# Kernel tuning notes

Hardware: AMD Instinct MI355X
Metric: run time of the kernel (lower is better)

## Reference

```python
import jax, jax.numpy as jnp
import numpy as np
import math

B, L, H = 2, 2048, 2048
NH, HD, RD = 16, 128, 64
QR, KVR = 768, 512


def rotate_half(x):
    d = x.shape[-1]
    x1, x2 = x[..., : d // 2], x[..., d // 2 :]
    return jnp.concatenate([-x2, x1], axis=-1)


def apply_rope(x):
    # x: [B, L, H, D] or [B, L, D]
    d = x.shape[-1]
    seq_len = x.shape[1]
    inv_freq = 1.0 / (10000.0 ** (jnp.arange(0, d, 2, dtype=x.dtype) / d))
    pos = jnp.arange(seq_len, dtype=x.dtype)
    freqs = jnp.outer(pos, inv_freq)  # [L, d/2]
    cos = jnp.concatenate([jnp.cos(freqs), jnp.cos(freqs)], axis=-1)  # [L, d]
    sin = jnp.concatenate([jnp.sin(freqs), jnp.sin(freqs)], axis=-1)
    if x.ndim == 4:
        cos, sin = cos[None, :, None, :], sin[None, :, None, :]
    else:
        cos, sin = cos[None, :, :], sin[None, :, :]
    return x * cos + rotate_half(x) * sin


def setup_inputs() -> dict:
    key = jax.random.key(0)
    ks = jax.random.split(key, 9)
    sc = lambda fan_in: 1.0 / math.sqrt(fan_in)
    return {
        "x": jax.random.normal(ks[0], (B, L, H), jnp.float32),
        "wq_down": jax.random.normal(ks[1], (H, QR), jnp.float32) * sc(H),
        "wq_up": jax.random.normal(ks[2], (QR, NH * HD), jnp.float32) * sc(QR),
        "wq_rope": jax.random.normal(ks[3], (QR, NH * RD), jnp.float32) * sc(QR),
        "wkv_down": jax.random.normal(ks[4], (H, KVR), jnp.float32) * sc(H),
        "wk_up": jax.random.normal(ks[5], (KVR, NH * HD), jnp.float32) * sc(KVR),
        "wv_up": jax.random.normal(ks[6], (KVR, NH * HD), jnp.float32) * sc(KVR),
        "wk_rope": jax.random.normal(ks[7], (H, RD), jnp.float32) * sc(H),
        "wo": jax.random.normal(ks[8], (NH * HD, H), jnp.float32) * sc(NH * HD),
    }


def reference(x, wq_down, wq_up, wq_rope, wkv_down, wk_up, wv_up, wk_rope, wo):
    b, l, _ = x.shape
    # Q low-rank path
    q_latent = x @ wq_down                              # [B,L,QR]
    q_content = (q_latent @ wq_up).reshape(b, l, NH, HD)
    q_rope = (q_latent @ wq_rope).reshape(b, l, NH, RD)
    q_rope = apply_rope(q_rope)
    # KV joint low-rank path
    kv_latent = x @ wkv_down                            # [B,L,KVR]
    k_content = (kv_latent @ wk_up).reshape(b, l, NH, HD)
    v = (kv_latent @ wv_up).reshape(b, l, NH, HD)
    # decoupled RoPE key (shared across heads)
    k_rope = apply_rope(x @ wk_rope)                    # [B,L,RD]
    k_rope = jnp.broadcast_to(k_rope[:, :, None, :], (b, l, NH, RD))
    q = jnp.concatenate([q_content, q_rope], axis=-1)   # [B,L,NH,HD+RD]
    k = jnp.concatenate([k_content, k_rope], axis=-1)
    scale = 1.0 / math.sqrt(HD + RD)
    scores = jnp.einsum("bqhd,bkhd->bhqk", q, k) * scale
    causal_mask = jnp.triu(jnp.ones((l, l), dtype=bool), k=1)
    scores = jnp.where(causal_mask[None, None], -jnp.inf, scores)
    attn = jax.nn.softmax(scores, axis=-1)
    out = jnp.einsum("bhqk,bkhd->bqhd", attn, v).reshape(b, l, NH * HD)
    return out @ wo
```

## Files before the change

### kernel.cpp

```cpp
#include <hip/hip_runtime.h>

typedef unsigned short u16;
typedef unsigned int u32;
typedef unsigned long long u64;
typedef __bf16 bf16x8 __attribute__((ext_vector_type(8)));
typedef float f32x4 __attribute__((ext_vector_type(4)));
typedef float f32x16 __attribute__((ext_vector_type(16)));
typedef u32 u32x4 __attribute__((ext_vector_type(4)));

#define DEV static __device__ __forceinline__

constexpr int B_ = 2, L_ = 2048, H_ = 2048;
constexpr int NH_ = 16, HD_ = 128, RD_ = 64;
constexpr int QR_ = 768, KVR_ = 512;
constexpr int BL_ = B_ * L_;
constexpr int QKD_ = HD_ + RD_;
constexpr int QKS_ = NH_ * QKD_;
constexpr int NHHD_ = NH_ * HD_;
constexpr int ROWS_ = B_ * NH_ * L_;
constexpr float SCALE2 = 0.07216878364870322f * 1.4426950408889634f;

DEV u16 f2bf(float f) {
    u32 u = __builtin_bit_cast(u32, f);
    u32 r = (u + 0x7fffu + ((u >> 16) & 1u)) >> 16;
    return (u16)r;
}
DEV float bf2f(u16 h) {
    u32 u = ((u32)h) << 16;
    return __builtin_bit_cast(float, u);
}
DEV u32 pk2(float lo, float hi) { return (u32)f2bf(lo) | ((u32)f2bf(hi) << 16); }
DEV bf16x8 ld8(const u16* p) { return __builtin_bit_cast(bf16x8, *(const u32x4*)p); }
DEV f32x4 mfma16(bf16x8 a, bf16x8 b, f32x4 c) {
    return __builtin_amdgcn_mfma_f32_16x16x32_bf16(a, b, c, 0, 0, 0);
}
DEV f32x16 mfma32(bf16x8 a, bf16x8 b, f32x16 c) {
    return __builtin_amdgcn_mfma_f32_32x32x16_bf16(a, b, c, 0, 0, 0);
}
DEV void gload16(const void* g, void* l) {
    __builtin_amdgcn_global_load_lds((const __attribute__((address_space(1))) void*)g,
                                     (__attribute__((address_space(3))) void*)l, 16, 0, 0);
}

__global__ __launch_bounds__(256) void cast_bf16_kernel(const float* __restrict__ src,
                                                        u16* __restrict__ dst, int n4) {
    int i = blockIdx.x * 256 + threadIdx.x;
    if (i >= n4) return;
    float4 v = ((const float4*)src)[i];
    u64 pk = (u64)f2bf(v.x) | ((u64)f2bf(v.y) << 16) | ((u64)f2bf(v.z) << 32) | ((u64)f2bf(v.w) << 48);
    ((u64*)dst)[i] = pk;
}

__global__ __launch_bounds__(256) void cast_transpose(const float* __restrict__ src, u16* __restrict__ dst,
                                                      int K, int N, int dstN) {
    __shared__ float tile[32][33];
    int n0 = blockIdx.x * 32, k0 = blockIdx.y * 32;
    int tx = threadIdx.x & 31, ty = threadIdx.x >> 5;
#pragma unroll
    for (int i = 0; i < 4; ++i) {
        int kk = ty + i * 8;
        int n = n0 + tx;
        tile[kk][tx] = (n < N) ? src[(size_t)(k0 + kk) * N + n] : 0.f;
    }
    __syncthreads();
#pragma unroll
    for (int i = 0; i < 4; ++i) {
        int nn = ty + i * 8;
        dst[(size_t)(n0 + nn) * K + k0 + tx] = f2bf(tile[tx][nn]);
    }
}

template <int OUTF32>
__global__ __launch_bounds__(256, 2) void gemm_bt(const u16* __restrict__ A, int lda,
                                                  const u16* __restrict__ Bt,
                                                  void* __restrict__ Cv, int ldc, int K) {
    __shared__ u16 As[128 * 32];
    __shared__ u16 Bs[128 * 32];
    const int tid = threadIdx.x;
    const int l = tid & 63, w = tid >> 6;
    const int l15 = l & 15, g = l >> 4;
    const int wr = w >> 1, wc = w & 1;
    const int bm = blockIdx.y * 128, bn = blockIdx.x * 128;

    const f32x4 zero = {0.f, 0.f, 0.f, 0.f};
    f32x4 acc[4][4];
#pragma unroll
    for (int m = 0; m < 4; ++m)
#pragma unroll
        for (int n = 0; n < 4; ++n) acc[m][n] = zero;

    const int ar0 = w * 32 + (l >> 2), kc8 = (l & 3) * 8;
    const u16* aptr = A + (size_t)(bm + ar0) * lda + kc8;
    const u16* aptr2 = A + (size_t)(bm + ar0 + 16) * lda + kc8;
    const u16* bptr = Bt + (size_t)(bn + ar0) * K + kc8;
    const u16* bptr2 = Bt + (size_t)(bn + ar0 + 16) * K + kc8;
    u16* asl = As + w * 1024;
    u16* bsl = Bs + w * 1024;

    const int nK = K / 32;
    for (int kt = 0; kt < nK; ++kt) {
        const int ko = kt * 32;
        __syncthreads();
        gload16(aptr + ko, asl);
        gload16(aptr2 + ko, asl + 512);
        gload16(bptr + ko, bsl);
        gload16(bptr2 + ko, bsl + 512);
        __syncthreads();
        bf16x8 af[4], bfr[4];
#pragma unroll
        for (int m = 0; m < 4; ++m)
            af[m] = ld8(As + (wr * 64 + m * 16 + l15) * 32 + g * 8);
#pragma unroll
        for (int n = 0; n < 4; ++n)
            bfr[n] = ld8(Bs + (wc * 64 + n * 16 + l15) * 32 + g * 8);
#pragma unroll
        for (int m = 0; m < 4; ++m)
#pragma unroll
            for (int n = 0; n < 4; ++n) acc[m][n] = mfma16(af[m], bfr[n], acc[m][n]);
    }
#pragma unroll
    for (int m = 0; m < 4; ++m)
#pragma unroll
        for (int n = 0; n < 4; ++n)
#pragma unroll
            for (int r = 0; r < 4; ++r) {
                int row = bm + wr * 64 + m * 16 + g * 4 + r;
                int col = bn + wc * 64 + n * 16 + l15;
                if (OUTF32)
                    ((float*)Cv)[(size_t)row * ldc + col] = acc[m][n][r];
                else
                    ((u16*)Cv)[(size_t)row * ldc + col] = f2bf(acc[m][n][r]);
            }
}

__global__ __launch_bounds__(256) void pack_content(const u16* __restrict__ src, int S,
                                                    u16* __restrict__ dst) {
    size_t i = (size_t)blockIdx.x * 256 + threadIdx.x;
    int token = (int)(i >> 8), c = (int)(i & 255);
    int h = c >> 4, d8 = c & 15;
    u32x4 v = *(const u32x4*)(src + (size_t)token * S + c * 8);
    *(u32x4*)(dst + (size_t)token * QKS_ + h * QKD_ + d8 * 8) = v;
}

__global__ __launch_bounds__(256) void rope_q_kernel(const u16* __restrict__ src, int S,
                                                     u16* __restrict__ dst) {
    int idx = blockIdx.x * 256 + threadIdx.x;
    int token = idx >> 9;
    int r = idx & 511;
    int h = r >> 5, i = r & 31;
    int pos = token & (L_ - 1);
    float ang = (float)pos * exp2f((float)i * (-13.287712379549449f / 32.f));
    float c = cosf(ang), s = sinf(ang);
    float x1 = bf2f(src[(size_t)token * S + h * 64 + i]);
    float x2 = bf2f(src[(size_t)token * S + h * 64 + i + 32]);
    u16* base = dst + (size_t)token * QKS_ + h * QKD_ + HD_;
    base[i] = f2bf(x1 * c - x2 * s);
    base[i + 32] = f2bf(x2 * c + x1 * s);
}

__global__ __launch_bounds__(256) void rope_k_kernel(const u16* __restrict__ src, int S,
                                                     u16* __restrict__ dst) {
    int idx = blockIdx.x * 256 + threadIdx.x;
    int token = idx >> 5, i = idx & 31;
    int pos = token & (L_ - 1);
    float ang = (float)pos * exp2f((float)i * (-13.287712379549449f / 32.f));
    float c = cosf(ang), s = sinf(ang);
    float x1 = bf2f(src[(size_t)token * S + i]);
    float x2 = bf2f(src[(size_t)token * S + i + 32]);
    u16 o1 = f2bf(x1 * c - x2 * s);
    u16 o2 = f2bf(x2 * c + x1 * s);
    u16* base = dst + (size_t)token * QKS_ + HD_;
#pragma unroll
    for (int h = 0; h < NH_; ++h) {
        base[h * QKD_ + i] = o1;
        base[h * QKD_ + i + 32] = o2;
    }
}

__global__ __launch_bounds__(256) void transpose_v(const u16* __restrict__ v, int S,
                                                   u16* __restrict__ vt) {
    __shared__ u16 tile[64][72];
    int cb = blockIdx.x * 64, lb = blockIdx.y * 64, b = blockIdx.z;
    int tid = threadIdx.x;
    int tr = tid >> 3, tc = (tid & 7) * 8;
#pragma unroll
    for (int i = 0; i < 2; ++i) {
        int row = tr + i * 32;
        u32x4 d = *(const u32x4*)(v + (size_t)(b * L_ + lb + row) * S + cb + tc);
        *(u32x4*)&tile[row][tc] = d;
    }
    __syncthreads();
#pragma unroll
    for (int i = 0; i < 2; ++i) {
        int col = tr + i * 32;
        u16 tmp[8];
#pragma unroll
        for (int j = 0; j < 8; ++j) tmp[j] = tile[tc + j][col];
        *(u32x4*)(vt + (size_t)(b * NHHD_ + cb + col) * L_ + lb + tc) = *(u32x4*)tmp;
    }
}

__global__ __launch_bounds__(256, 2) void flash_attn(const u16* __restrict__ q, const u16* __restrict__ k,
                                                     const u16* __restrict__ vt,
                                                     float* __restrict__ opart, float* __restrict__ mlpart) {
    __shared__ __align__(16) u16 Ks[2][64 * 192];
    __shared__ __align__(16) u16 Vs[2][128 * 64];
    const int p = blockIdx.x >> 1, split = blockIdx.x & 1;
    const int h = blockIdx.y, b = blockIdx.z;
    const int tid = threadIdx.x, w = tid >> 6, l = tid & 63;
    const int ql = l & 31, hi = l >> 5;
    const int sw = ql & 7;

    const u16* kbase = k + (size_t)(b * L_) * QKS_ + h * QKD_;
    const u16* vtbase = vt + (size_t)(b * NHHD_ + h * HD_) * L_;

    int koff[6], voff[4];
#pragma unroll
    for (int j = 0; j < 6; ++j) {
        int off = j * 4096 + tid * 16;
        int row = off / 384;
        int gr = (off % 384) / 16;
        koff[j] = row * QKS_ + (gr ^ (row & 7)) * 8;
    }
#pragma unroll
    for (int j = 0; j < 4; ++j) {
        int off = j * 4096 + tid * 16;
        int row = off >> 7;
        int gr = (off >> 4) & 7;
        voff[j] = row * L_ + (gr ^ (row & 7)) * 8;
    }

    auto STAGE = [&](int buf, int kv0) {
        const u16* kb = kbase + (size_t)kv0 * QKS_;
#pragma unroll
        for (int j = 0; j < 6; ++j)
            gload16(kb + koff[j], (u16*)Ks[buf] + j * 2048 + w * 512);
        const u16* vb = vtbase + kv0;
#pragma unroll
        for (int j = 0; j < 4; ++j)
            gload16(vb + voff[j], (u16*)Vs[buf] + j * 2048 + w * 512);
    };

    for (int half = 0; half < 2; ++half) {
        const int qtile = half ? 15 - p : p;
        const int q0 = qtile * 128;
        const int qabs = q0 + w * 32 + ql;

        bf16x8 qf[12];
        {
            const u16* qrow = q + (size_t)(b * L_ + qabs) * QKS_ + h * QKD_;
#pragma unroll
            for (int c = 0; c < 12; ++c) qf[c] = ld8(qrow + c * 16 + hi * 8);
        }
        f32x16 o[4];
#pragma unroll
        for (int n = 0; n < 4; ++n)
#pragma unroll
            for (int r = 0; r < 16; ++r) o[n][r] = 0.f;
        float m2 = -1e30f, lsum = 0.f;

        const int nt = 2 * qtile + 2;
        __syncthreads();
        STAGE(0, split * 64);
        int i = 0;
        for (int t = split; t < nt; t += 2, ++i) {
            __syncthreads();
            if (t + 2 < nt) STAGE((i + 1) & 1, (t + 2) * 64);
            const u16* Kb = Ks[i & 1];
            const u16* Vb = Vs[i & 1];
            const int kv0 = t * 64;

            f32x16 s0, s1;
#pragma unroll
            for (int r = 0; r < 16; ++r) { s0[r] = 0.f; s1[r] = 0.f; }
#pragma unroll
            for (int c = 0; c < 12; ++c) {
                int gsw = ((2 * c + hi) ^ sw) * 16;
                bf16x8 k0 = ld8((const u16*)((const char*)Kb + ql * 384 + gsw));
                bf16x8 k1 = ld8((const u16*)((const char*)Kb + (32 + ql) * 384 + gsw));
                s0 = mfma32(k0, qf[c], s0);
                s1 = mfma32(k1, qf[c], s1);
            }

            const bool domask = (kv0 + 63 > q0);
            float mx = -3e38f;
#pragma unroll
            for (int r = 0; r < 16; ++r) {
                const int kk = (r & 3) + 8 * (r >> 2) + 4 * hi;
                float x0 = s0[r] * SCALE2;
                float x1 = s1[r] * SCALE2;
                if (domask) {
                    if (kv0 + kk > qabs) x0 = -3e38f;
                    if (kv0 + 32 + kk > qabs) x1 = -3e38f;
                }
                s0[r] = x0; s1[r] = x1;
                mx = fmaxf(mx, fmaxf(x0, x1));
            }
            mx = fmaxf(mx, __shfl_xor(mx, 32));
            const float mnew = fmaxf(m2, mx);
            const float f = exp2f(m2 - mnew);
            m2 = mnew;
            float sl = 0.f;
#pragma unroll
            for (int r = 0; r < 16; ++r) {
                float p0 = exp2f(s0[r] - m2);
                float p1 = exp2f(s1[r] - m2);
                s0[r] = p0; s1[r] = p1;
                sl += p0 + p1;
            }
            lsum = lsum * f + sl;
#pragma unroll
            for (int n = 0; n < 4; ++n)
#pragma unroll
                for (int r = 0; r < 16; ++r) o[n][r] *= f;

#pragma unroll
            for (int c = 0; c < 4; ++c) {
                const int rb = 8 * (c & 1);
                float p0, p1, p2, p3, p4, p5, p6, p7;
                if (c < 2) {
                    p0 = s0[rb + 0]; p1 = s0[rb + 1]; p2 = s0[rb + 2]; p3 = s0[rb + 3];
                    p4 = s0[rb + 4]; p5 = s0[rb + 5]; p6 = s0[rb + 6]; p7 = s0[rb + 7];
                } else {
                    p0 = s1[rb + 0]; p1 = s1[rb + 1]; p2 = s1[rb + 2]; p3 = s1[rb + 3];
                    p4 = s1[rb + 4]; p5 = s1[rb + 5]; p6 = s1[rb + 6]; p7 = s1[rb + 7];
                }
                u32 a0 = pk2(p0, p1), a1 = pk2(p2, p3);
                u32 b0 = pk2(p4, p5), b1 = pk2(p6, p7);
                u32 pa0 = (u32)__shfl_xor((int)a0, 32);
                u32 pa1 = (u32)__shfl_xor((int)a1, 32);
                u32 pb0 = (u32)__shfl_xor((int)b0, 32);
                u32 pb1 = (u32)__shfl_xor((int)b1, 32);
                u32x4 pw = {hi ? pb0 : a0, hi ? pb1 : a1, hi ? b0 : pa0, hi ? b1 : pa1};
                bf16x8 pf = __builtin_bit_cast(bf16x8, pw);
                const int gsw = ((2 * c + hi) ^ sw) * 16;
#pragma unroll
                for (int n = 0; n < 4; ++n) {
                    bf16x8 vf = ld8((const u16*)((const char*)Vb + (32 * n + ql) * 128 + gsw));
                    o[n] = mfma32(vf, pf, o[n]);
                }
            }
        }

        const float ltot = lsum + __shfl_xor(lsum, 32);
        const int row = ((b * NH_ + h) << 11) + qabs;
        float* ob = opart + ((size_t)split * ROWS_ + row) * 128;
#pragma unroll
        for (int n = 0; n < 4; ++n)
#pragma unroll
            for (int rg = 0; rg < 4; ++rg) {
                f32x4 v = {o[n][4 * rg + 0], o[n][4 * rg + 1], o[n][4 * rg + 2], o[n][4 * rg + 3]};
                *(f32x4*)(ob + 32 * n + 8 * rg + 4 * hi) = v;
            }
        if (!hi) {
            float2 ml = {m2, ltot};
            *(float2*)(mlpart + ((size_t)split * ROWS_ + row) * 2) = ml;
        }
    }
}

__global__ __launch_bounds__(256) void combine_attn(const float* __restrict__ opart,
                                                    const float* __restrict__ mlpart,
                                                    u16* __restrict__ attn_o) {
    int idx = blockIdx.x * 256 + threadIdx.x;
    int row = idx >> 5, dq = (idx & 31) * 4;
    float2 ml0 = *(const float2*)(mlpart + (size_t)row * 2);
    float2 ml1 = *(const float2*)(mlpart + ((size_t)ROWS_ + row) * 2);
    float m = fmaxf(ml0.x, ml1.x);
    float w0 = exp2f(ml0.x - m), w1 = exp2f(ml1.x - m);
    float inv = 1.f / (w0 * ml0.y + w1 * ml1.y);
    w0 *= inv; w1 *= inv;
    f32x4 a = *(const f32x4*)(opart + (size_t)row * 128 + dq);
    f32x4 c = *(const f32x4*)(opart + ((size_t)ROWS_ + row) * 128 + dq);
    int b = row >> 15, h = (row >> 11) & 15, qrow = row & 2047;
    u16* dst = attn_o + (size_t)(b * L_ + qrow) * NHHD_ + h * HD_ + dq;
    u64 pk = (u64)pk2(a[0] * w0 + c[0] * w1, a[1] * w0 + c[1] * w1) |
             ((u64)pk2(a[2] * w0 + c[2] * w1, a[3] * w0 + c[3] * w1) << 32);
    *(u64*)dst = pk;
}

extern "C" void kernel_launch(void* const* d_in, const int* in_sizes, int n_in,
                              void* d_out, int out_size, void* d_ws, size_t ws_size,
                              hipStream_t stream) {
    (void)in_sizes; (void)n_in; (void)out_size; (void)ws_size;
    const float* x = (const float*)d_in[0];
    const float* wq_down = (const float*)d_in[1];
    const float* wq_up = (const float*)d_in[2];
    const float* wq_rope = (const float*)d_in[3];
    const float* wkv_down = (const float*)d_in[4];
    const float* wk_up = (const float*)d_in[5];
    const float* wv_up = (const float*)d_in[6];
    const float* wk_rope = (const float*)d_in[7];
    const float* wo = (const float*)d_in[8];

    u16* W = (u16*)d_ws;
    size_t off = 0;
    auto alloc = [&](size_t e) { u16* p = W + off; off += (e + 127) & ~(size_t)127; return p; };

    u16* xb    = alloc((size_t)BL_ * H_);
    u16* Wdn   = alloc((size_t)1408 * H_);
    u16* Wupq  = alloc((size_t)3072 * QR_);
    u16* Wupkv = alloc((size_t)4096 * KVR_);
    u16* Wo_t  = alloc((size_t)H_ * NHHD_);
    u16* C1    = alloc((size_t)BL_ * 1408);
    u16* C2    = alloc((size_t)BL_ * 3072);
    u16* C3    = alloc((size_t)BL_ * 4096);
    u16* qbuf  = alloc((size_t)BL_ * QKS_);
    u16* kbuf  = alloc((size_t)BL_ * QKS_);
    u16* vt    = alloc((size_t)BL_ * NHHD_);
    u16* attn_o = alloc((size_t)BL_ * NHHD_);

    float* opart  = (float*)C1;
    float* mlpart = opart + (size_t)2 * ROWS_ * 128;

    cast_bf16_kernel<<<(BL_ * H_ / 4 + 255) / 256, 256, 0, stream>>>(x, xb, BL_ * H_ / 4);
    cast_transpose<<<dim3(QR_ / 32, H_ / 32), 256, 0, stream>>>(wq_down, Wdn, H_, QR_, QR_);
    cast_transpose<<<dim3(KVR_ / 32, H_ / 32), 256, 0, stream>>>(wkv_down, Wdn + (size_t)768 * H_, H_, KVR_, KVR_);
    cast_transpose<<<dim3(128 / 32, H_ / 32), 256, 0, stream>>>(wk_rope, Wdn + (size_t)1280 * H_, H_, RD_, 128);
    cast_transpose<<<dim3(NHHD_ / 32, QR_ / 32), 256, 0, stream>>>(wq_up, Wupq, QR_, NHHD_, NHHD_);
    cast_transpose<<<dim3(1024 / 32, QR_ / 32), 256, 0, stream>>>(wq_rope, Wupq + (size_t)2048 * QR_, QR_, 1024, 1024);
    cast_transpose<<<dim3(NHHD_ / 32, KVR_ / 32), 256, 0, stream>>>(wk_up, Wupkv, KVR_, NHHD_, NHHD_);
    cast_transpose<<<dim3(NHHD_ / 32, KVR_ / 32), 256, 0, stream>>>(wv_up, Wupkv + (size_t)2048 * KVR_, KVR_, NHHD_, NHHD_);
    cast_transpose<<<dim3(NHHD_ / 32, H_ / 32), 256, 0, stream>>>(wo, Wo_t, NHHD_, H_, H_);

    gemm_bt<0><<<dim3(1408 / 128, BL_ / 128), 256, 0, stream>>>(xb, H_, Wdn, C1, 1408, H_);
    gemm_bt<0><<<dim3(3072 / 128, BL_ / 128), 256, 0, stream>>>(C1, 1408, Wupq, C2, 3072, QR_);
    gemm_bt<0><<<dim3(4096 / 128, BL_ / 128), 256, 0, stream>>>(C1 + 768, 1408, Wupkv, C3, 4096, KVR_);

    pack_content<<<BL_ * NHHD_ / 8 / 256, 256, 0, stream>>>(C2, 3072, qbuf);
    pack_content<<<BL_ * NHHD_ / 8 / 256, 256, 0, stream>>>(C3, 4096, kbuf);
    rope_q_kernel<<<BL_ * NH_ * 32 / 256, 256, 0, stream>>>(C2 + 2048, 3072, qbuf);
    rope_k_kernel<<<BL_ * 32 / 256, 256, 0, stream>>>(C1 + 1280, 1408, kbuf);
    transpose_v<<<dim3(NHHD_ / 64, L_ / 64, B_), 256, 0, stream>>>(C3 + 2048, 4096, vt);

    flash_attn<<<dim3(16, NH_, B_), 256, 0, stream>>>(qbuf, kbuf, vt, opart, mlpart);
    combine_attn<<<ROWS_ * 32 / 256, 256, 0, stream>>>(opart, mlpart, attn_o);

    gemm_bt<1><<<dim3(H_ / 128, BL_ / 128), 256, 0, stream>>>(attn_o, NHHD_, Wo_t, d_out, H_, NHHD_);
}
```

Before: 329.8 us.

## Fuse pack, RoPE and V transpose into GEMM epilogues; tweak attention softmax

Folds the Q/K content packing, Q RoPE (scale folded in) and the V transpose into specialized GEMM epilogues. This removes several elementwise kernels and their intermediate buffers. It also doubles the GEMM K-tile to 64, precomputes a RoPE cos/sin table, uses native bf16 conversion, and adds setprio around the MFMA loops. In flash attention it skips rescaling unless the max grows past a threshold (lazy rescale). This adds numerical risk if the threshold bounds are off, and more LDS per GEMM block.

```diff
diff --git a/kernel.cpp b/kernel.cpp
--- a/kernel.cpp
+++ b/kernel.cpp
@@ -21,9 +21,8 @@
 constexpr float SCALE2 = 0.07216878364870322f * 1.4426950408889634f;
 
 DEV u16 f2bf(float f) {
-    u32 u = __builtin_bit_cast(u32, f);
-    u32 r = (u + 0x7fffu + ((u >> 16) & 1u)) >> 16;
-    return (u16)r;
+    __bf16 h = (__bf16)f;
+    return __builtin_bit_cast(u16, h);
 }
 DEV float bf2f(u16 h) {
     u32 u = ((u32)h) << 16;
@@ -70,12 +69,21 @@
     }
 }
 
-template <int OUTF32>
+__global__ __launch_bounds__(256) void build_rope_tab(float2* __restrict__ tab) {
+    int idx = blockIdx.x * 256 + threadIdx.x;
+    int pos = idx >> 5, i = idx & 31;
+    float freq = exp2f((float)i * (-13.287712379549449f / 32.f));
+    float ang = (float)pos * freq;
+    tab[idx] = make_float2(cosf(ang), sinf(ang));
+}
+
+template <int EPI>
 __global__ __launch_bounds__(256, 2) void gemm_bt(const u16* __restrict__ A, int lda,
                                                   const u16* __restrict__ Bt,
-                                                  void* __restrict__ Cv, int ldc, int K) {
-    __shared__ u16 As[128 * 32];
-    __shared__ u16 Bs[128 * 32];
+                                                  void* __restrict__ Cv, void* __restrict__ Cv2,
+                                                  int ldc, int K, const float2* __restrict__ tab) {
+    __shared__ u16 As[128 * 64];
+    __shared__ u16 Bs[128 * 64];
     const int tid = threadIdx.x;
     const int l = tid & 63, w = tid >> 6;
     const int l15 = l & 15, g = l >> 4;
@@ -89,114 +97,140 @@
 #pragma unroll
         for (int n = 0; n < 4; ++n) acc[m][n] = zero;
 
-    const int ar0 = w * 32 + (l >> 2), kc8 = (l & 3) * 8;
-    const u16* aptr = A + (size_t)(bm + ar0) * lda + kc8;
-    const u16* aptr2 = A + (size_t)(bm + ar0 + 16) * lda + kc8;
-    const u16* bptr = Bt + (size_t)(bn + ar0) * K + kc8;
-    const u16* bptr2 = Bt + (size_t)(bn + ar0 + 16) * K + kc8;
-    u16* asl = As + w * 1024;
-    u16* bsl = Bs + w * 1024;
-
-    const int nK = K / 32;
+    int aoff[4], boff[4];
+#pragma unroll
+    for (int j = 0; j < 4; ++j) {
+        int chunk = j * 256 + tid;
+        int row = chunk >> 3, gr = chunk & 7;
+        aoff[j] = row * lda + gr * 8;
+        boff[j] = row * K + gr * 8;
+    }
+    const u16* Ab = A + (size_t)bm * lda;
+    const u16* Bb = Bt + (size_t)bn * K;
+
+    const int nK = K / 64;
     for (int kt = 0; kt < nK; ++kt) {
-        const int ko = kt * 32;
+        const int ko = kt * 64;
         __syncthreads();
-        gload16(aptr + ko, asl);
-        gload16(aptr2 + ko, asl + 512);
-        gload16(bptr + ko, bsl);
-        gload16(bptr2 + ko, bsl + 512);
+#pragma unroll
+        for (int j = 0; j < 4; ++j) gload16(Ab + ko + aoff[j], As + j * 2048 + w * 512);
+#pragma unroll
+        for (int j = 0; j < 4; ++j) gload16(Bb + ko + boff[j], Bs + j * 2048 + w * 512);
         __syncthreads();
-        bf16x8 af[4], bfr[4];
+#pragma unroll
+        for (int kk = 0; kk < 2; ++kk) {
+            bf16x8 af[4], bfr[4];
+#pragma unroll
+            for (int m = 0; m < 4; ++m)
+                af[m] = ld8(As + (wr * 64 + m * 16 + l15) * 64 + kk * 32 + g * 8);
+#pragma unroll
+            for (int n = 0; n < 4; ++n)
+                bfr[n] = ld8(Bs + (wc * 64 + n * 16 + l15) * 64 + kk * 32 + g * 8);
+#pragma unroll
+            for (int m = 0; m < 4; ++m)
+#pragma unroll
+                for (int n = 0; n < 4; ++n) acc[m][n] = mfma16(af[m], bfr[n], acc[m][n]);
+        }
+    }
+
+    if constexpr (EPI == 0 || EPI == 1) {
 #pragma unroll
         for (int m = 0; m < 4; ++m)
-            af[m] = ld8(As + (wr * 64 + m * 16 + l15) * 32 + g * 8);
-#pragma unroll
-        for (int n = 0; n < 4; ++n)
-            bfr[n] = ld8(Bs + (wc * 64 + n * 16 + l15) * 32 + g * 8);
-#pragma unroll
-        for (int m = 0; m < 4; ++m)
-#pragma unroll
-            for (int n = 0; n < 4; ++n) acc[m][n] = mfma16(af[m], bfr[n], acc[m][n]);
-    }
-#pragma unroll
-    for (int m = 0; m < 4; ++m)
-#pragma unroll
-        for (int n = 0; n < 4; ++n)
-#pragma unroll
-            for (int r = 0; r < 4; ++r) {
-                int row = bm + wr * 64 + m * 16 + g * 4 + r;
-                int col = bn + wc * 64 + n * 16 + l15;
-                if (OUTF32)
-                    ((float*)Cv)[(size_t)row * ldc + col] = acc[m][n][r];
-                else
-                    ((u16*)Cv)[(size_t)row * ldc + col] = f2bf(acc[m][n][r]);
-            }
-}
-
-__global__ __launch_bounds__(256) void pack_content(const u16* __restrict__ src, int S,
-                                                    u16* __restrict__ dst) {
-    size_t i = (size_t)blockIdx.x * 256 + threadIdx.x;
-    int token = (int)(i >> 8), c = (int)(i & 255);
-    int h = c >> 4, d8 = c & 15;
-    u32x4 v = *(const u32x4*)(src + (size_t)token * S + c * 8);
-    *(u32x4*)(dst + (size_t)token * QKS_ + h * QKD_ + d8 * 8) = v;
-}
-
-__global__ __launch_bounds__(256) void rope_q_kernel(const u16* __restrict__ src, int S,
-                                                     u16* __restrict__ dst) {
-    int idx = blockIdx.x * 256 + threadIdx.x;
-    int token = idx >> 9;
-    int r = idx & 511;
-    int h = r >> 5, i = r & 31;
-    int pos = token & (L_ - 1);
-    float ang = (float)pos * exp2f((float)i * (-13.287712379549449f / 32.f));
-    float c = cosf(ang), s = sinf(ang);
-    float x1 = bf2f(src[(size_t)token * S + h * 64 + i]);
-    float x2 = bf2f(src[(size_t)token * S + h * 64 + i + 32]);
-    u16* base = dst + (size_t)token * QKS_ + h * QKD_ + HD_;
-    base[i] = f2bf(x1 * c - x2 * s);
-    base[i + 32] = f2bf(x2 * c + x1 * s);
+#pragma unroll
+            for (int n = 0; n < 4; ++n)
+#pragma unroll
+                for (int r = 0; r < 4; ++r) {
+                    int row = bm + wr * 64 + m * 16 + g * 4 + r;
+                    int col = bn + wc * 64 + n * 16 + l15;
+                    if (EPI == 1)
+                        ((float*)Cv)[(size_t)row * ldc + col] = acc[m][n][r];
+                    else
+                        ((u16*)Cv)[(size_t)row * ldc + col] = f2bf(acc[m][n][r]);
+                }
+    }
+    if constexpr (EPI == 2) {
+        const int base = bn + wc * 64;
+        u16* qb = (u16*)Cv;
+        if (base < 2048) {
+            const int h = base >> 7, dbase = base & 127;
+#pragma unroll
+            for (int m = 0; m < 4; ++m)
+#pragma unroll
+                for (int n = 0; n < 4; ++n)
+#pragma unroll
+                    for (int r = 0; r < 4; ++r) {
+                        int token = bm + wr * 64 + m * 16 + g * 4 + r;
+                        qb[(size_t)token * QKS_ + h * QKD_ + dbase + n * 16 + l15] =
+                            f2bf(acc[m][n][r] * SCALE2);
+                    }
+        } else {
+            const int h = (base - 2048) >> 6;
+#pragma unroll
+            for (int m = 0; m < 4; ++m)
+#pragma unroll
+                for (int r = 0; r < 4; ++r) {
+                    const int token = bm + wr * 64 + m * 16 + g * 4 + r;
+                    const int pos = token & (L_ - 1);
+                    u16* bp = qb + (size_t)token * QKS_ + h * QKD_ + HD_;
+#pragma unroll
+                    for (int n = 0; n < 2; ++n) {
+                        const int i = n * 16 + l15;
+                        float2 cs = tab[pos * 32 + i];
+                        float x1 = acc[m][n][r], x2 = acc[m][n + 2][r];
+                        bp[i] = f2bf((x1 * cs.x - x2 * cs.y) * SCALE2);
+                        bp[i + 32] = f2bf((x2 * cs.x + x1 * cs.y) * SCALE2);
+                    }
+                }
+        }
+    }
+    if constexpr (EPI == 3) {
+        const int base = bn + wc * 64;
+        if (base < 2048) {
+            u16* kb = (u16*)Cv;
+            const int h = base >> 7, dbase = base & 127;
+#pragma unroll
+            for (int m = 0; m < 4; ++m)
+#pragma unroll
+                for (int n = 0; n < 4; ++n)
+#pragma unroll
+                    for (int r = 0; r < 4; ++r) {
+                        int token = bm + wr * 64 + m * 16 + g * 4 + r;
+                        kb[(size_t)token * QKS_ + h * QKD_ + dbase + n * 16 + l15] =
+                            f2bf(acc[m][n][r]);
+                    }
+        } else {
+            u16* vtb = (u16*)Cv2;
+            const int b = bm >> 11;
+#pragma unroll
+            for (int m = 0; m < 4; ++m)
+#pragma unroll
+                for (int n = 0; n < 4; ++n) {
+                    const int vc = base - 2048 + n * 16 + l15;
+                    const int qrow = (bm + wr * 64 + m * 16 + g * 4) & (L_ - 1);
+                    u64 pk = (u64)pk2(acc[m][n][0], acc[m][n][1]) |
+                             ((u64)pk2(acc[m][n][2], acc[m][n][3]) << 32);
+                    *(u64*)(vtb + (size_t)(b * NHHD_ + vc) * L_ + qrow) = pk;
+                }
+        }
+    }
 }
 
 __global__ __launch_bounds__(256) void rope_k_kernel(const u16* __restrict__ src, int S,
-                                                     u16* __restrict__ dst) {
+                                                     u16* __restrict__ dst,
+                                                     const float2* __restrict__ tab) {
     int idx = blockIdx.x * 256 + threadIdx.x;
     int token = idx >> 5, i = idx & 31;
     int pos = token & (L_ - 1);
-    float ang = (float)pos * exp2f((float)i * (-13.287712379549449f / 32.f));
-    float c = cosf(ang), s = sinf(ang);
+    float2 cs = tab[pos * 32 + i];
     float x1 = bf2f(src[(size_t)token * S + i]);
     float x2 = bf2f(src[(size_t)token * S + i + 32]);
-    u16 o1 = f2bf(x1 * c - x2 * s);
-    u16 o2 = f2bf(x2 * c + x1 * s);
+    u16 o1 = f2bf(x1 * cs.x - x2 * cs.y);
+    u16 o2 = f2bf(x2 * cs.x + x1 * cs.y);
     u16* base = dst + (size_t)token * QKS_ + HD_;
 #pragma unroll
     for (int h = 0; h < NH_; ++h) {
         base[h * QKD_ + i] = o1;
         base[h * QKD_ + i + 32] = o2;
-    }
-}
-
-__global__ __launch_bounds__(256) void transpose_v(const u16* __restrict__ v, int S,
-                                                   u16* __restrict__ vt) {
-    __shared__ u16 tile[64][72];
-    int cb = blockIdx.x * 64, lb = blockIdx.y * 64, b = blockIdx.z;
-    int tid = threadIdx.x;
-    int tr = tid >> 3, tc = (tid & 7) * 8;
-#pragma unroll
-    for (int i = 0; i < 2; ++i) {
-        int row = tr + i * 32;
-        u32x4 d = *(const u32x4*)(v + (size_t)(b * L_ + lb + row) * S + cb + tc);
-        *(u32x4*)&tile[row][tc] = d;
-    }
-    __syncthreads();
-#pragma unroll
-    for (int i = 0; i < 2; ++i) {
-        int col = tr + i * 32;
-        u16 tmp[8];
-#pragma unroll
-        for (int j = 0; j < 8; ++j) tmp[j] = tile[tc + j][col];
-        *(u32x4*)(vt + (size_t)(b * NHHD_ + cb + col) * L_ + lb + tc) = *(u32x4*)tmp;
     }
 }
 
@@ -273,6 +307,7 @@
             f32x16 s0, s1;
 #pragma unroll
             for (int r = 0; r < 16; ++r) { s0[r] = 0.f; s1[r] = 0.f; }
+            __builtin_amdgcn_s_setprio(1);
 #pragma unroll
             for (int c = 0; c < 12; ++c) {
                 int gsw = ((2 * c + hi) ^ sw) * 16;
@@ -281,25 +316,34 @@
                 s0 = mfma32(k0, qf[c], s0);
                 s1 = mfma32(k1, qf[c], s1);
             }
+            __builtin_amdgcn_s_setprio(0);
 
             const bool domask = (kv0 + 63 > q0);
             float mx = -3e38f;
 #pragma unroll
             for (int r = 0; r < 16; ++r) {
                 const int kk = (r & 3) + 8 * (r >> 2) + 4 * hi;
-                float x0 = s0[r] * SCALE2;
-                float x1 = s1[r] * SCALE2;
+                float x0 = s0[r];
+                float x1 = s1[r];
                 if (domask) {
                     if (kv0 + kk > qabs) x0 = -3e38f;
                     if (kv0 + 32 + kk > qabs) x1 = -3e38f;
-                }
-                s0[r] = x0; s1[r] = x1;
+                    s0[r] = x0; s1[r] = x1;
+                }
                 mx = fmaxf(mx, fmaxf(x0, x1));
             }
             mx = fmaxf(mx, __shfl_xor(mx, 32));
-            const float mnew = fmaxf(m2, mx);
-            const float f = exp2f(m2 - mnew);
-            m2 = mnew;
+
+            if (__any(mx > m2 + 8.f)) {
+                const float f = exp2f(m2 - fmaxf(m2, mx));
+                m2 = fmaxf(m2, mx);
+                lsum *= f;
+#pragma unroll
+                for (int n = 0; n < 4; ++n)
+#pragma unroll
+                    for (int r = 0; r < 16; ++r) o[n][r] *= f;
+            }
+
             float sl = 0.f;
 #pragma unroll
             for (int r = 0; r < 16; ++r) {
@@ -308,11 +352,7 @@
                 s0[r] = p0; s1[r] = p1;
                 sl += p0 + p1;
             }
-            lsum = lsum * f + sl;
-#pragma unroll
-            for (int n = 0; n < 4; ++n)
-#pragma unroll
-                for (int r = 0; r < 16; ++r) o[n][r] *= f;
+            lsum += sl;
 
 #pragma unroll
             for (int c = 0; c < 4; ++c) {
@@ -334,11 +374,13 @@
                 u32x4 pw = {hi ? pb0 : a0, hi ? pb1 : a1, hi ? b0 : pa0, hi ? b1 : pa1};
                 bf16x8 pf = __builtin_bit_cast(bf16x8, pw);
                 const int gsw = ((2 * c + hi) ^ sw) * 16;
+                __builtin_amdgcn_s_setprio(1);
 #pragma unroll
                 for (int n = 0; n < 4; ++n) {
                     bf16x8 vf = ld8((const u16*)((const char*)Vb + (32 * n + ql) * 128 + gsw));
                     o[n] = mfma32(vf, pf, o[n]);
                 }
+                __builtin_amdgcn_s_setprio(0);
             }
         }
 
@@ -402,14 +444,16 @@
     u16* Wupq  = alloc((size_t)3072 * QR_);
     u16* Wupkv = alloc((size_t)4096 * KVR_);
     u16* Wo_t  = alloc((size_t)H_ * NHHD_);
+    u16* tabm  = alloc((size_t)L_ * 32 * 4);
     u16* C1    = alloc((size_t)BL_ * 1408);
-    u16* C2    = alloc((size_t)BL_ * 3072);
-    u16* C3    = alloc((size_t)BL_ * 4096);
+    u16* pad_  = alloc((size_t)28311552);
     u16* qbuf  = alloc((size_t)BL_ * QKS_);
     u16* kbuf  = alloc((size_t)BL_ * QKS_);
     u16* vt    = alloc((size_t)BL_ * NHHD_);
     u16* attn_o = alloc((size_t)BL_ * NHHD_);
-
+    (void)pad_;
+
+    float2* tab = (float2*)tabm;
     float* opart  = (float*)C1;
     float* mlpart = opart + (size_t)2 * ROWS_ * 128;
 
@@ -422,19 +466,16 @@
     cast_transpose<<<dim3(NHHD_ / 32, KVR_ / 32), 256, 0, stream>>>(wk_up, Wupkv, KVR_, NHHD_, NHHD_);
     cast_transpose<<<dim3(NHHD_ / 32, KVR_ / 32), 256, 0, stream>>>(wv_up, Wupkv + (size_t)2048 * KVR_, KVR_, NHHD_, NHHD_);
     cast_transpose<<<dim3(NHHD_ / 32, H_ / 32), 256, 0, stream>>>(wo, Wo_t, NHHD_, H_, H_);
-
-    gemm_bt<0><<<dim3(1408 / 128, BL_ / 128), 256, 0, stream>>>(xb, H_, Wdn, C1, 1408, H_);
-    gemm_bt<0><<<dim3(3072 / 128, BL_ / 128), 256, 0, stream>>>(C1, 1408, Wupq, C2, 3072, QR_);
-    gemm_bt<0><<<dim3(4096 / 128, BL_ / 128), 256, 0, stream>>>(C1 + 768, 1408, Wupkv, C3, 4096, KVR_);
-
-    pack_content<<<BL_ * NHHD_ / 8 / 256, 256, 0, stream>>>(C2, 3072, qbuf);
-    pack_content<<<BL_ * NHHD_ / 8 / 256, 256, 0, stream>>>(C3, 4096, kbuf);
-    rope_q_kernel<<<BL_ * NH_ * 32 / 256, 256, 0, stream>>>(C2 + 2048, 3072, qbuf);
-    rope_k_kernel<<<BL_ * 32 / 256, 256, 0, stream>>>(C1 + 1280, 1408, kbuf);
-    transpose_v<<<dim3(NHHD_ / 64, L_ / 64, B_), 256, 0, stream>>>(C3 + 2048, 4096, vt);
+    build_rope_tab<<<L_ * 32 / 256, 256, 0, stream>>>(tab);
+
+    gemm_bt<0><<<dim3(1408 / 128, BL_ / 128), 256, 0, stream>>>(xb, H_, Wdn, C1, nullptr, 1408, H_, nullptr);
+    gemm_bt<2><<<dim3(3072 / 128, BL_ / 128), 256, 0, stream>>>(C1, 1408, Wupq, qbuf, nullptr, 0, QR_, tab);
+    gemm_bt<3><<<dim3(4096 / 128, BL_ / 128), 256, 0, stream>>>(C1 + 768, 1408, Wupkv, kbuf, vt, 0, KVR_, nullptr);
+
+    rope_k_kernel<<<BL_ * 32 / 256, 256, 0, stream>>>(C1 + 1280, 1408, kbuf, tab);
 
     flash_attn<<<dim3(16, NH_, B_), 256, 0, stream>>>(qbuf, kbuf, vt, opart, mlpart);
     combine_attn<<<ROWS_ * 32 / 256, 256, 0, stream>>>(opart, mlpart, attn_o);
 
-    gemm_bt<1><<<dim3(H_ / 128, BL_ / 128), 256, 0, stream>>>(attn_o, NHHD_, Wo_t, d_out, H_, NHHD_);
-}
+    gemm_bt<1><<<dim3(H_ / 128, BL_ / 128), 256, 0, stream>>>(attn_o, NHHD_, Wo_t, d_out, nullptr, H_, NHHD_, nullptr);
+}
```

Measured after the change: 546.5 us. +65.7%, slower.
